# Performance work log

Hardware: AMD Instinct MI355X
Metric: run time of the kernel (lower is better)

## Reference

```python
import jax, jax.numpy as jnp
import numpy as np

N = 50000      # nodes
E = 800000     # edges (before self loops)
H = 4          # heads
C = 32         # hidden_channels per head
HC = H * C     # 128
L = 3          # num_layers - 2 conv blocks
G = 128        # graphs in batch
OUT = 10       # out_channels
VOCAB = 100
EPS = 1e-5


def setup_inputs() -> dict:
    key = jax.random.key(0)
    ks = jax.random.split(key, 16)
    s = 0.1
    return {
        "x_idx": jax.random.randint(ks[0], (N,), 0, VOCAB),
        "edge_index": jax.random.randint(ks[1], (2, E), 0, N),
        "batch": jnp.sort(jax.random.randint(ks[2], (N,), 0, G)),
        "embed": jax.random.normal(ks[3], (VOCAB, HC), jnp.float32) * s,
        "bn_gamma": jnp.ones((L, HC), jnp.float32),
        "bn_beta": jnp.zeros((L, HC), jnp.float32),
        "lin_W": jax.random.normal(ks[4], (L, C, HC), jnp.float32) * s,   # maps HC -> C (hidden)
        "lin_b": jnp.zeros((L, C), jnp.float32),
        "gat_W": jax.random.normal(ks[5], (L, HC, C), jnp.float32) * s,   # maps C -> H*C
        "att_src": jax.random.normal(ks[6], (L, H, C), jnp.float32) * s,
        "att_dst": jax.random.normal(ks[7], (L, H, C), jnp.float32) * s,
        "gat_b": jnp.zeros((L, HC), jnp.float32),
        "readout_W": jax.random.normal(ks[8], (OUT, HC), jnp.float32) * s,
        "readout_b": jnp.zeros((OUT,), jnp.float32),
    }


def _segment_softmax(logits, seg, num_segments):
    # logits: [E, H], seg: [E]
    m = jax.ops.segment_max(logits, seg, num_segments=num_segments)
    m = jnp.where(jnp.isfinite(m), m, 0.0)
    e = jnp.exp(logits - m[seg])
    z = jax.ops.segment_sum(e, seg, num_segments=num_segments)
    return e / (z[seg] + 1e-16)


def _forward(x_idx, edge_index, batch, embed, bn_gamma, bn_beta, lin_W, lin_b,
             gat_W, att_src, att_dst, gat_b, readout_W, readout_b):
    x = embed[x_idx]                                   # [N, HC]
    loops = jnp.arange(N)
    src = jnp.concatenate([edge_index[0], loops])      # add_self_loops=True
    dst = jnp.concatenate([edge_index[1], loops])
    for l in range(L):
        # BatchNorm1d (batch statistics)
        mean = jnp.mean(x, axis=0)
        var = jnp.var(x, axis=0)
        x = bn_gamma[l] * (x - mean) * jax.lax.rsqrt(var + EPS) + bn_beta[l]
        # Linear(HC -> C) + relu; dropout = identity (eval)
        x = jax.nn.relu(x @ lin_W[l].T + lin_b[l])      # [N, C]
        # GATConv(C -> C, heads=H, concat)
        h = (x @ gat_W[l].T).reshape(N, H, C)           # [N, H, C]
        a_src = jnp.sum(h * att_src[l], axis=-1)        # [N, H]
        a_dst = jnp.sum(h * att_dst[l], axis=-1)        # [N, H]
        logits = jax.nn.leaky_relu(a_src[src] + a_dst[dst], 0.2)  # [E+N, H]
        alpha = _segment_softmax(logits, dst, N)        # softmax over in-edges of each dst
        msg = h[src] * alpha[:, :, None]                # [E+N, H, C]
        x = jax.ops.segment_sum(msg, dst, num_segments=N).reshape(N, HC) + gat_b[l]
    x = x @ readout_W.T + readout_b                     # [N, OUT]
    return jax.ops.segment_sum(x, batch, num_segments=G)  # [G, OUT]


def reference(x_idx, edge_index, batch, embed, bn_gamma, bn_beta, lin_W, lin_b,
              gat_W, att_src, att_dst, gat_b, readout_W, readout_b):
    return _forward(x_idx, edge_index, batch, embed, bn_gamma, bn_beta, lin_W, lin_b,
                    gat_W, att_src, att_dst, gat_b, readout_W, readout_b)
```

## Files before the change

kernel.cpp:

```cpp
#include <hip/hip_runtime.h>

constexpr int NN   = 50000;
constexpr int NE   = 800000;
constexpr int NHD  = 4;
constexpr int CC   = 32;
constexpr int HCC  = 128;
constexpr int NL   = 3;
constexpr int NG   = 128;
constexpr int NOUT = 10;
constexpr float BN_EPS = 1e-5f;

constexpr int X2S = 67;
constexpr int YS = 33;
constexpr int NSLOT = 64;
constexpr int NBUK = (NN + 127) / 128;
constexpr int EB  = 2048;

__device__ inline unsigned f2bf_pack(float a, float b) {
    unsigned ua = __float_as_uint(a); ua += 0x7FFFu + ((ua >> 16) & 1u);
    unsigned ub = __float_as_uint(b); ub += 0x7FFFu + ((ub >> 16) & 1u);
    return (ua >> 16) | (ub & 0xFFFF0000u);
}
__device__ inline float bf_lo(unsigned p) { return __uint_as_float(p << 16); }
__device__ inline float bf_hi(unsigned p) { return __uint_as_float(p & 0xFFFF0000u); }

__global__ __launch_bounds__(256) void k_embed_stats(const int* __restrict__ idx,
                                                     const float* __restrict__ embed,
                                                     unsigned* __restrict__ xp,
                                                     float* __restrict__ stats) {
    int tid = threadIdx.x;
    int i0 = blockIdx.x * 256 + tid;
    int stride = gridDim.x * 256;
    float s0 = 0.f, s1 = 0.f, q0 = 0.f, q1 = 0.f;
    for (int i = i0; i < NN * 64; i += stride) {
        int n = i >> 6, c2 = (i & 63) << 1;
        float2 ev = *(const float2*)(embed + (size_t)idx[n] * HCC + c2);
        xp[i] = f2bf_pack(ev.x, ev.y);
        s0 += ev.x; q0 += ev.x * ev.x;
        s1 += ev.y; q1 += ev.y * ev.y;
    }
    __shared__ float A[256], B[256], C[256], D[256];
    A[tid] = s0; B[tid] = s1; C[tid] = q0; D[tid] = q1;
    __syncthreads();
    int slot = blockIdx.x & (NSLOT - 1);
    if (tid < 64) {
        int p = tid;
        float S0 = A[p] + A[p + 64] + A[p + 128] + A[p + 192];
        float S1 = B[p] + B[p + 64] + B[p + 128] + B[p + 192];
        float Q0 = C[p] + C[p + 64] + C[p + 128] + C[p + 192];
        float Q1 = D[p] + D[p + 64] + D[p + 128] + D[p + 192];
        atomicAdd(&stats[slot * 256 + 2 * p],           S0);
        atomicAdd(&stats[slot * 256 + 2 * p + 1],       S1);
        atomicAdd(&stats[slot * 256 + HCC + 2 * p],     Q0);
        atomicAdd(&stats[slot * 256 + HCC + 2 * p + 1], Q1);
    }
}

__global__ __launch_bounds__(256) void k_bhist(const int* __restrict__ ei,
                                               int* __restrict__ bkcnt,
                                               const int* __restrict__ batch,
                                               float* __restrict__ gcnt) {
    __shared__ int hist[NBUK];
    __shared__ int lgc[NG];
    int b = blockIdx.x, t = threadIdx.x;
    int e0 = b * EB, nE = min(EB, NE - e0);
    for (int i = t; i < NBUK; i += 256) hist[i] = 0;
    for (int i = t; i < NG; i += 256) lgc[i] = 0;
    __syncthreads();
    for (int i = t; i < nE; i += 256)
        atomicAdd(&hist[ei[NE + e0 + i] >> 7], 1);
    int n0 = b * 128;
    if (t < 128) {
        int n = n0 + t;
        if (n < NN) atomicAdd(&lgc[batch[n]], 1);
    }
    __syncthreads();
    for (int i = t; i < NBUK; i += 256)
        if (hist[i]) atomicAdd(&bkcnt[i], hist[i]);
    for (int i = t; i < NG; i += 256)
        if (lgc[i]) atomicAdd(&gcnt[i], (float)lgc[i]);
}

__global__ __launch_bounds__(512) void k_bscan(const int* __restrict__ bkcnt,
                                               int* __restrict__ bbase,
                                               int* __restrict__ bcnt,
                                               int* __restrict__ rowptr) {
    __shared__ int sc[512];
    int t = threadIdx.x;
    int v = (t < NBUK) ? bkcnt[t] : 0;
    sc[t] = v;
    __syncthreads();
#pragma unroll
    for (int off = 1; off < 512; off <<= 1) {
        int u = (t >= off) ? sc[t - off] : 0;
        __syncthreads();
        sc[t] += u;
        __syncthreads();
    }
    if (t < NBUK) {
        int excl = sc[t] - v;
        bbase[t] = excl;
        bcnt[t]  = excl;
    }
    if (t == 0) rowptr[NN] = NE;
}

__global__ __launch_bounds__(256) void k_bin(const int* __restrict__ ei,
                                             int* __restrict__ bcnt,
                                             unsigned* __restrict__ e_src) {
    __shared__ int hist[NBUK], base[NBUK];
    int b = blockIdx.x, t = threadIdx.x;
    int e0 = b * EB;
    int nE = min(EB, NE - e0);

    for (int i = t; i < NBUK; i += 256) hist[i] = 0;
    __syncthreads();
    for (int i = t; i < nE; i += 256)
        atomicAdd(&hist[ei[NE + e0 + i] >> 7], 1);
    __syncthreads();
    for (int i = t; i < NBUK; i += 256) {
        int c = hist[i];
        if (c) base[i] = atomicAdd(&bcnt[i], c);
        hist[i] = 0;
    }
    __syncthreads();
    for (int i = t; i < nE; i += 256) {
        int e = e0 + i;
        int d = ei[NE + e];
        int s = ei[e];
        int bk = d >> 7;
        int pos = base[bk] + atomicAdd(&hist[bk], 1);
        e_src[pos] = (unsigned)s | ((unsigned)(d & 127) << 17);
    }
}

__global__ __launch_bounds__(512) void k_place(const int* __restrict__ bbase,
                                               unsigned* __restrict__ e_src,
                                               int* __restrict__ rowptr) {
    __shared__ int lcnt[128], sc[128], lrp[128], cnt[128];
    int b = blockIdx.x, t = threadIdx.x;
    int d0 = b * 128;
    int rS = bbase[b];
    int rE = (b + 1 < NBUK) ? bbase[b + 1] : NE;
    int n = rE - rS;
    if (t < 128) { lcnt[t] = 0; cnt[t] = 0; }
    __syncthreads();
    unsigned pk[7];
#pragma unroll
    for (int k = 0; k < 7; k++) {
        int i = t + k * 512;
        if (i < n) {
            pk[k] = e_src[rS + i];
            atomicAdd(&lcnt[pk[k] >> 17], 1);
        }
    }
    __syncthreads();
    if (t < 128) sc[t] = lcnt[t];
    __syncthreads();
#pragma unroll
    for (int off = 1; off < 128; off <<= 1) {
        int u = (t < 128 && t >= off) ? sc[t - off] : 0;
        __syncthreads();
        if (t < 128) sc[t] += u;
        __syncthreads();
    }
    if (t < 128) {
        int start = rS + sc[t] - lcnt[t];
        lrp[t] = start;
        int d = d0 + t;
        if (d < NN) rowptr[d] = start;
    }
    __syncthreads();
#pragma unroll
    for (int k = 0; k < 7; k++) {
        int i = t + k * 512;
        if (i < n) {
            unsigned p = pk[k];
            int dl = p >> 17;
            int pos = lrp[dl] + atomicAdd(&cnt[dl], 1);
            e_src[pos] = p & 0x1FFFFu;
        }
    }
}

__global__ __launch_bounds__(256) void k_fused(const unsigned* __restrict__ xp,
                                               const float* __restrict__ stats,
                                               const float* __restrict__ gamma,
                                               const float* __restrict__ beta,
                                               const float* __restrict__ W1,
                                               const float* __restrict__ b1,
                                               const float* __restrict__ W2,
                                               const float* __restrict__ aS,
                                               const float* __restrict__ aD,
                                               unsigned* __restrict__ h,
                                               float* __restrict__ asrc,
                                               float* __restrict__ adst) {
    __shared__ unsigned xb2[64 * X2S];
    __shared__ float yt[64 * YS];
    __shared__ float __attribute__((aligned(16))) ssl[256];
    int tid = threadIdx.x;
    int node0 = blockIdx.x * 64;
    int nNodes = min(64, NN - node0);

    if (tid < 128) {
        float s = 0.f, q = 0.f;
        for (int sl = 0; sl < NSLOT; sl++) {
            s += stats[sl * 256 + tid];
            q += stats[sl * 256 + HCC + tid];
        }
        float mean = s * (1.0f / NN);
        float var  = q * (1.0f / NN) - mean * mean;
        float sc   = gamma[tid] * rsqrtf(var + BN_EPS);
        ssl[tid]       = sc;
        ssl[HCC + tid] = beta[tid] - mean * sc;
    }
    __syncthreads();

    {
        for (int q4 = tid; q4 < nNodes * 16; q4 += 256) {
            int n = q4 >> 4, c8 = q4 & 15;
            uint4 xv = *(const uint4*)(xp + (size_t)(node0 + n) * 64 + c8 * 4);
            int c = c8 * 8;
            float4 sc0 = *(const float4*)&ssl[c];
            float4 sc1 = *(const float4*)&ssl[c + 4];
            float4 sh0 = *(const float4*)&ssl[HCC + c];
            float4 sh1 = *(const float4*)&ssl[HCC + c + 4];
            unsigned* dst = &xb2[n * X2S + c8 * 4];
            dst[0] = f2bf_pack(bf_lo(xv.x) * sc0.x + sh0.x, bf_hi(xv.x) * sc0.y + sh0.y);
            dst[1] = f2bf_pack(bf_lo(xv.y) * sc0.z + sh0.z, bf_hi(xv.y) * sc0.w + sh0.w);
            dst[2] = f2bf_pack(bf_lo(xv.z) * sc1.x + sh1.x, bf_hi(xv.z) * sc1.y + sh1.y);
            dst[3] = f2bf_pack(bf_lo(xv.w) * sc1.z + sh1.z, bf_hi(xv.w) * sc1.w + sh1.w);
        }
    }
    __syncthreads();

    int lane = tid & 63;
    int wv = __builtin_amdgcn_readfirstlane(tid >> 6);
    int n = lane;

    {
        int j0 = wv * 8;
        const float* w1p = W1 + j0 * 128;
        float acc[8];
#pragma unroll
        for (int k = 0; k < 8; k++) acc[k] = b1[j0 + k];
        if (n < nNodes) {
            for (int cb = 0; cb < 128; cb += 4) {
                unsigned p0 = xb2[n * X2S + (cb >> 1)];
                unsigned p1 = xb2[n * X2S + (cb >> 1) + 1];
                float xv0 = bf_lo(p0), xv1 = bf_hi(p0);
                float xv2 = bf_lo(p1), xv3 = bf_hi(p1);
#pragma unroll
                for (int k = 0; k < 8; k++) {
                    float4 w = *(const float4*)&w1p[k * 128 + cb];
                    acc[k] += xv0 * w.x + xv1 * w.y + xv2 * w.z + xv3 * w.w;
                }
            }
#pragma unroll
            for (int k = 0; k < 8; k++) yt[n * YS + j0 + k] = fmaxf(acc[k], 0.f);
        }
    }
    __syncthreads();

    if (n < nNodes) {
        int k0 = wv * 32, hd = wv;
        const float* w2p = W2 + k0 * 32;
        const float* aSp = aS + hd * 32;
        const float* aDp = aD + hd * 32;
        float yreg[32];
#pragma unroll
        for (int j = 0; j < 32; j++) yreg[j] = yt[n * YS + j];
        float sa = 0.f, da = 0.f;
        unsigned* hrow = h + (size_t)(node0 + n) * 64;
        for (int kb = 0; kb < 32; kb += 8) {
            float acck[8];
#pragma unroll
            for (int kk = 0; kk < 8; kk++) acck[kk] = 0.f;
#pragma unroll
            for (int j = 0; j < 32; j += 4) {
#pragma unroll
                for (int kk = 0; kk < 8; kk++) {
                    float4 w = *(const float4*)&w2p[(kb + kk) * 32 + j];
                    acck[kk] += yreg[j] * w.x + yreg[j + 1] * w.y +
                                yreg[j + 2] * w.z + yreg[j + 3] * w.w;
                }
            }
#pragma unroll
            for (int kk = 0; kk < 8; kk++) {
                sa += acck[kk] * aSp[kb + kk];
                da += acck[kk] * aDp[kb + kk];
            }
            uint4 pk;
            pk.x = f2bf_pack(acck[0], acck[1]);
            pk.y = f2bf_pack(acck[2], acck[3]);
            pk.z = f2bf_pack(acck[4], acck[5]);
            pk.w = f2bf_pack(acck[6], acck[7]);
            *(uint4*)(hrow + ((kb) >> 1) + (k0 >> 1)) = pk;
        }
        asrc[(node0 + n) * 4 + hd] = sa;
        adst[(node0 + n) * 4 + hd] = da;
    }
}

__global__ __launch_bounds__(256) void k_agg(const int* __restrict__ rowptr,
                                             const int* __restrict__ e_src,
                                             const float* __restrict__ asrc,
                                             const float* __restrict__ adst,
                                             const unsigned* __restrict__ h,
                                             const float* __restrict__ gat_b,
                                             unsigned* __restrict__ xo,
                                             float* __restrict__ stats,
                                             const int* __restrict__ batch,
                                             float* __restrict__ gsum,
                                             int mode) {
    int tid = threadIdx.x, lane = tid & 63, wv = tid >> 6;
    int g  = lane >> 4;
    int li = lane & 15;
    int hd = li >> 2;
    int d  = blockIdx.x * 16 + wv * 4 + g;

    float4 bA = *(const float4*)(gat_b + li * 8);
    float4 bB = *(const float4*)(gat_b + li * 8 + 4);

    int begin = rowptr[d];
    int end   = rowptr[d + 1];
    float adv = adst[d * 4 + hd];
    float asl = asrc[d * 4 + hd];
    uint4 hs  = *(const uint4*)(h + (size_t)d * 64 + li * 4);

    float acc[8];
#pragma unroll
    for (int k = 0; k < 8; k++) acc[k] = 0.f;
    float ws = 0.f;

    int s[8];
    if (begin < end) {
#pragma unroll
        for (int t = 0; t < 8; t++) s[t] = e_src[min(begin + t, end - 1)];
    }

    for (int j = begin; j < end; j += 8) {
        uint4 hv[8];
#pragma unroll
        for (int t = 0; t < 8; t++) hv[t] = *(const uint4*)(h + (size_t)s[t] * 64 + li * 4);
        float av[8];
#pragma unroll
        for (int t = 0; t < 8; t++) av[t] = asrc[s[t] * 4 + hd];
        int jn = j + 8;
        int sn[8];
#pragma unroll
        for (int t = 0; t < 8; t++) sn[t] = s[t];
        if (jn < end) {
#pragma unroll
            for (int t = 0; t < 8; t++) sn[t] = e_src[min(jn + t, end - 1)];
        }
#pragma unroll
        for (int t = 0; t < 8; t++) {
            float l = av[t] + adv; l = l > 0.f ? l : 0.2f * l;
            float w = (j + t < end) ? __expf(l) : 0.f;
            acc[0] += w * bf_lo(hv[t].x); acc[1] += w * bf_hi(hv[t].x);
            acc[2] += w * bf_lo(hv[t].y); acc[3] += w * bf_hi(hv[t].y);
            acc[4] += w * bf_lo(hv[t].z); acc[5] += w * bf_hi(hv[t].z);
            acc[6] += w * bf_lo(hv[t].w); acc[7] += w * bf_hi(hv[t].w);
            ws += w;
        }
#pragma unroll
        for (int t = 0; t < 8; t++) s[t] = sn[t];
    }

    {
        float l = asl + adv; l = l > 0.f ? l : 0.2f * l;
        float w = __expf(l);
        acc[0] += w * bf_lo(hs.x); acc[1] += w * bf_hi(hs.x);
        acc[2] += w * bf_lo(hs.y); acc[3] += w * bf_hi(hs.y);
        acc[4] += w * bf_lo(hs.z); acc[5] += w * bf_hi(hs.z);
        acc[6] += w * bf_lo(hs.w); acc[7] += w * bf_hi(hs.w);
        ws += w;
    }

    float inv = 1.0f / (ws + 1e-16f);
    float o[8];
    o[0] = acc[0] * inv + bA.x; o[1] = acc[1] * inv + bA.y;
    o[2] = acc[2] * inv + bA.z; o[3] = acc[3] * inv + bA.w;
    o[4] = acc[4] * inv + bB.x; o[5] = acc[5] * inv + bB.y;
    o[6] = acc[6] * inv + bB.z; o[7] = acc[7] * inv + bB.w;

    __shared__ float redS[16 * 128], redQ[16 * 128];
    __shared__ int bg[16];
    int r = wv * 4 + g;

    if (mode == 1) {
        uint4 pk;
        pk.x = f2bf_pack(o[0], o[1]);
        pk.y = f2bf_pack(o[2], o[3]);
        pk.z = f2bf_pack(o[4], o[5]);
        pk.w = f2bf_pack(o[6], o[7]);
        *(uint4*)(xo + (size_t)d * 64 + li * 4) = pk;

#pragma unroll
        for (int k = 0; k < 8; k++) {
            redS[r * 128 + li * 8 + k] = o[k];
            redQ[r * 128 + li * 8 + k] = o[k] * o[k];
        }
        __syncthreads();
        int slot = blockIdx.x & (NSLOT - 1);
        if (tid < 128) {
            float v = 0.f;
#pragma unroll
            for (int rr = 0; rr < 16; rr++) v += redS[rr * 128 + tid];
            atomicAdd(&stats[slot * 256 + tid], v);
        } else {
            int c = tid - 128;
            float v = 0.f;
#pragma unroll
            for (int rr = 0; rr < 16; rr++) v += redQ[rr * 128 + c];
            atomicAdd(&stats[slot * 256 + HCC + c], v);
        }
    } else {
        if (li == 0) bg[r] = batch[d];
#pragma unroll
        for (int k = 0; k < 8; k++) redS[r * 128 + li * 8 + k] = o[k];
        __syncthreads();
        if (tid < 128) {
            float sacc = 0.f;
            int curg = bg[0];
#pragma unroll
            for (int rr = 0; rr < 16; rr++) {
                int gg = bg[rr];
                if (gg != curg) {
                    atomicAdd(&gsum[curg * HCC + tid], sacc);
                    sacc = 0.f; curg = gg;
                }
                sacc += redS[rr * 128 + tid];
            }
            atomicAdd(&gsum[curg * HCC + tid], sacc);
        }
    }
}

__global__ __launch_bounds__(128) void k_out(const float* __restrict__ gsum,
                                             const float* __restrict__ gcnt,
                                             const float* __restrict__ W,
                                             const float* __restrict__ bb,
                                             float* __restrict__ out) {
    __shared__ float v[128];
    int g = blockIdx.x, t = threadIdx.x;
    v[t] = gsum[g * HCC + t];
    __syncthreads();
    if (t < NOUT) {
        float acc = gcnt[g] * bb[t];
        const float* wr = W + t * HCC;
        for (int c = 0; c < HCC; c++) acc += v[c] * wr[c];
        out[g * NOUT + t] = acc;
    }
}

extern "C" void kernel_launch(void* const* d_in, const int* in_sizes, int n_in,
                              void* d_out, int out_size, void* d_ws, size_t ws_size,
                              hipStream_t stream) {
    const int*   x_idx = (const int*)d_in[0];
    const int*   ei    = (const int*)d_in[1];
    const int*   batch = (const int*)d_in[2];
    const float* embed = (const float*)d_in[3];
    const float* bn_g  = (const float*)d_in[4];
    const float* bn_b  = (const float*)d_in[5];
    const float* lin_W = (const float*)d_in[6];
    const float* lin_b = (const float*)d_in[7];
    const float* gat_W = (const float*)d_in[8];
    const float* att_s = (const float*)d_in[9];
    const float* att_d = (const float*)d_in[10];
    const float* gat_b = (const float*)d_in[11];
    const float* ro_W  = (const float*)d_in[12];
    const float* ro_b  = (const float*)d_in[13];
    float* out = (float*)d_out;

    const size_t STG = (size_t)NSLOT * 256;
    unsigned* xp    = (unsigned*)d_ws;
    unsigned* h     = xp + (size_t)NN * 64;
    float*    asrc  = (float*)(h + (size_t)NN * 64);
    float*    adst  = asrc + (size_t)NN * NHD;
    float*    stats = adst + (size_t)NN * NHD;
    float*    gsum  = stats + 3 * STG;
    float*    gcnt  = gsum + (size_t)NG * HCC;
    int*      bkcnt  = (int*)(gcnt + NG);
    int*      bbase  = bkcnt + NBUK;
    int*      bcnt   = bbase + NBUK;
    int*      rowptr = bcnt + NBUK;
    unsigned* e_src  = (unsigned*)(rowptr + NN + 1);

    hipMemsetAsync(stats, 0,
                   (3 * STG + (size_t)NG * HCC + NG) * sizeof(float) + NBUK * sizeof(int),
                   stream);

    k_embed_stats<<<512, 256, 0, stream>>>(x_idx, embed, xp, stats);
    k_bhist<<<(NE + EB - 1) / EB, 256, 0, stream>>>(ei, bkcnt, batch, gcnt);
    k_bscan<<<1, 512, 0, stream>>>(bkcnt, bbase, bcnt, rowptr);
    k_bin<<<(NE + EB - 1) / EB, 256, 0, stream>>>(ei, bcnt, e_src);
    k_place<<<NBUK, 512, 0, stream>>>(bbase, e_src, rowptr);

    for (int l = 0; l < NL; ++l) {
        k_fused<<<(NN + 63) / 64, 256, 0, stream>>>(xp, stats + l * STG,
                                                    bn_g + l * HCC, bn_b + l * HCC,
                                                    lin_W + l * CC * HCC, lin_b + l * CC,
                                                    gat_W + l * HCC * CC,
                                                    att_s + l * NHD * CC,
                                                    att_d + l * NHD * CC,
                                                    h, asrc, adst);
        k_agg<<<NN / 16, 256, 0, stream>>>(rowptr, (const int*)e_src, asrc, adst, h,
                                           gat_b + l * HCC, xp,
                                           stats + (l + 1) * STG,
                                           batch, gsum,
                                           (l < NL - 1) ? 1 : 2);
    }

    k_out<<<NG, 128, 0, stream>>>(gsum, gcnt, ro_W, ro_b, out);
}
```

Measured before the change: 338.3 us.

## Sort each node's in-edges into source-range tiles and aggregate tile by tile

During CSR construction, each destination's edges are now grouped into four source-index ranges (12500 nodes each), and per-node counts for each range are stored in a new tcnt array. The aggregation kernel walks these four segments in order with an unroll of 4 instead of 8. The aim is temporal locality in the h/asrc gathers: all waves sweep source ranges in a similar order, so the working set in L2 is smaller. The cost is an extra per-node count read, more loop overhead and tail waste per segment, and less memory-level parallelism from the smaller unroll.

```diff
diff --git a/kernel.cpp b/kernel.cpp
--- a/kernel.cpp
+++ b/kernel.cpp
@@ -15,6 +15,8 @@
 constexpr int NSLOT = 64;
 constexpr int NBUK = (NN + 127) / 128;
 constexpr int EB  = 2048;
+constexpr int NT  = 4;
+constexpr int TSZ = 12500;
 
 __device__ inline unsigned f2bf_pack(float a, float b) {
     unsigned ua = __float_as_uint(a); ua += 0x7FFFu + ((ua >> 16) & 1u);
@@ -136,26 +138,37 @@
 
 __global__ __launch_bounds__(512) void k_place(const int* __restrict__ bbase,
                                                unsigned* __restrict__ e_src,
-                                               int* __restrict__ rowptr) {
-    __shared__ int lcnt[128], sc[128], lrp[128], cnt[128];
+                                               int* __restrict__ rowptr,
+                                               int* __restrict__ tcnt) {
+    __shared__ int lcnt2[128][NT], cnt2[128][NT], sc[128], lrp[128];
     int b = blockIdx.x, t = threadIdx.x;
     int d0 = b * 128;
     int rS = bbase[b];
     int rE = (b + 1 < NBUK) ? bbase[b + 1] : NE;
     int n = rE - rS;
-    if (t < 128) { lcnt[t] = 0; cnt[t] = 0; }
-    __syncthreads();
-    unsigned pk[7];
+    if (t < 128) {
+#pragma unroll
+        for (int k = 0; k < NT; k++) { lcnt2[t][k] = 0; cnt2[t][k] = 0; }
+    }
+    __syncthreads();
+    unsigned pk[7]; int tl[7];
 #pragma unroll
     for (int k = 0; k < 7; k++) {
         int i = t + k * 512;
         if (i < n) {
             pk[k] = e_src[rS + i];
-            atomicAdd(&lcnt[pk[k] >> 17], 1);
-        }
-    }
-    __syncthreads();
-    if (t < 128) sc[t] = lcnt[t];
+            int src = pk[k] & 0x1FFFFu;
+            tl[k] = min(src / TSZ, NT - 1);
+            atomicAdd(&lcnt2[pk[k] >> 17][tl[k]], 1);
+        }
+    }
+    __syncthreads();
+    int deg = 0;
+    if (t < 128) {
+#pragma unroll
+        for (int k = 0; k < NT; k++) deg += lcnt2[t][k];
+        sc[t] = deg;
+    }
     __syncthreads();
 #pragma unroll
     for (int off = 1; off < 128; off <<= 1) {
@@ -165,10 +178,16 @@
         __syncthreads();
     }
     if (t < 128) {
-        int start = rS + sc[t] - lcnt[t];
+        int start = rS + sc[t] - deg;
         lrp[t] = start;
         int d = d0 + t;
-        if (d < NN) rowptr[d] = start;
+        if (d < NN) {
+            rowptr[d] = start;
+            *(int4*)&tcnt[(size_t)d * NT] =
+                make_int4(lcnt2[t][0], lcnt2[t][1], lcnt2[t][2], lcnt2[t][3]);
+        }
+        int b0 = 0, b1 = lcnt2[t][0], b2 = b1 + lcnt2[t][1], b3 = b2 + lcnt2[t][2];
+        lcnt2[t][0] = b0; lcnt2[t][1] = b1; lcnt2[t][2] = b2; lcnt2[t][3] = b3;
     }
     __syncthreads();
 #pragma unroll
@@ -177,7 +196,7 @@
         if (i < n) {
             unsigned p = pk[k];
             int dl = p >> 17;
-            int pos = lrp[dl] + atomicAdd(&cnt[dl], 1);
+            int pos = lrp[dl] + lcnt2[dl][tl[k]] + atomicAdd(&cnt2[dl][tl[k]], 1);
             e_src[pos] = p & 0x1FFFFu;
         }
     }
@@ -304,6 +323,7 @@
 
 __global__ __launch_bounds__(256) void k_agg(const int* __restrict__ rowptr,
                                              const int* __restrict__ e_src,
+                                             const int* __restrict__ tcnt,
                                              const float* __restrict__ asrc,
                                              const float* __restrict__ adst,
                                              const unsigned* __restrict__ h,
@@ -323,49 +343,56 @@
     float4 bB = *(const float4*)(gat_b + li * 8 + 4);
 
     int begin = rowptr[d];
-    int end   = rowptr[d + 1];
     float adv = adst[d * 4 + hd];
     float asl = asrc[d * 4 + hd];
     uint4 hs  = *(const uint4*)(h + (size_t)d * 64 + li * 4);
+    int tcs[4];
+    {
+        int4 tc = *(const int4*)(tcnt + (size_t)d * 4);
+        tcs[0] = tc.x; tcs[1] = tc.y; tcs[2] = tc.z; tcs[3] = tc.w;
+    }
 
     float acc[8];
 #pragma unroll
     for (int k = 0; k < 8; k++) acc[k] = 0.f;
     float ws = 0.f;
 
-    int s[8];
-    if (begin < end) {
-#pragma unroll
-        for (int t = 0; t < 8; t++) s[t] = e_src[min(begin + t, end - 1)];
-    }
-
-    for (int j = begin; j < end; j += 8) {
-        uint4 hv[8];
-#pragma unroll
-        for (int t = 0; t < 8; t++) hv[t] = *(const uint4*)(h + (size_t)s[t] * 64 + li * 4);
-        float av[8];
-#pragma unroll
-        for (int t = 0; t < 8; t++) av[t] = asrc[s[t] * 4 + hd];
-        int jn = j + 8;
-        int sn[8];
-#pragma unroll
-        for (int t = 0; t < 8; t++) sn[t] = s[t];
-        if (jn < end) {
-#pragma unroll
-            for (int t = 0; t < 8; t++) sn[t] = e_src[min(jn + t, end - 1)];
-        }
-#pragma unroll
-        for (int t = 0; t < 8; t++) {
-            float l = av[t] + adv; l = l > 0.f ? l : 0.2f * l;
-            float w = (j + t < end) ? __expf(l) : 0.f;
-            acc[0] += w * bf_lo(hv[t].x); acc[1] += w * bf_hi(hv[t].x);
-            acc[2] += w * bf_lo(hv[t].y); acc[3] += w * bf_hi(hv[t].y);
-            acc[4] += w * bf_lo(hv[t].z); acc[5] += w * bf_hi(hv[t].z);
-            acc[6] += w * bf_lo(hv[t].w); acc[7] += w * bf_hi(hv[t].w);
-            ws += w;
-        }
-#pragma unroll
-        for (int t = 0; t < 8; t++) s[t] = sn[t];
+    int segB = begin;
+    for (int tt = 0; tt < NT; ++tt) {
+        int sB = segB, sE = segB + tcs[tt];
+        segB = sE;
+        if (sB >= sE) continue;
+        int s[4];
+#pragma unroll
+        for (int t = 0; t < 4; t++) s[t] = e_src[min(sB + t, sE - 1)];
+        for (int j = sB; j < sE; j += 4) {
+            uint4 hv[4];
+#pragma unroll
+            for (int t = 0; t < 4; t++) hv[t] = *(const uint4*)(h + (size_t)s[t] * 64 + li * 4);
+            float av[4];
+#pragma unroll
+            for (int t = 0; t < 4; t++) av[t] = asrc[s[t] * 4 + hd];
+            int jn = j + 4;
+            int sn[4];
+#pragma unroll
+            for (int t = 0; t < 4; t++) sn[t] = s[t];
+            if (jn < sE) {
+#pragma unroll
+                for (int t = 0; t < 4; t++) sn[t] = e_src[min(jn + t, sE - 1)];
+            }
+#pragma unroll
+            for (int t = 0; t < 4; t++) {
+                float l = av[t] + adv; l = l > 0.f ? l : 0.2f * l;
+                float w = (j + t < sE) ? __expf(l) : 0.f;
+                acc[0] += w * bf_lo(hv[t].x); acc[1] += w * bf_hi(hv[t].x);
+                acc[2] += w * bf_lo(hv[t].y); acc[3] += w * bf_hi(hv[t].y);
+                acc[4] += w * bf_lo(hv[t].z); acc[5] += w * bf_hi(hv[t].z);
+                acc[6] += w * bf_lo(hv[t].w); acc[7] += w * bf_hi(hv[t].w);
+                ws += w;
+            }
+#pragma unroll
+            for (int t = 0; t < 4; t++) s[t] = sn[t];
+        }
     }
 
     {
@@ -487,6 +514,7 @@
     int*      bcnt   = bbase + NBUK;
     int*      rowptr = bcnt + NBUK;
     unsigned* e_src  = (unsigned*)(rowptr + NN + 1);
+    int*      tcnt   = (int*)((((size_t)(e_src + NE)) + 15) & ~(size_t)15);
 
     hipMemsetAsync(stats, 0,
                    (3 * STG + (size_t)NG * HCC + NG) * sizeof(float) + NBUK * sizeof(int),
@@ -496,7 +524,7 @@
     k_bhist<<<(NE + EB - 1) / EB, 256, 0, stream>>>(ei, bkcnt, batch, gcnt);
     k_bscan<<<1, 512, 0, stream>>>(bkcnt, bbase, bcnt, rowptr);
     k_bin<<<(NE + EB - 1) / EB, 256, 0, stream>>>(ei, bcnt, e_src);
-    k_place<<<NBUK, 512, 0, stream>>>(bbase, e_src, rowptr);
+    k_place<<<NBUK, 512, 0, stream>>>(bbase, e_src, rowptr, tcnt);
 
     for (int l = 0; l < NL; ++l) {
         k_fused<<<(NN + 63) / 64, 256, 0, stream>>>(xp, stats + l * STG,
@@ -506,7 +534,7 @@
                                                     att_s + l * NHD * CC,
                                                     att_d + l * NHD * CC,
                                                     h, asrc, adst);
-        k_agg<<<NN / 16, 256, 0, stream>>>(rowptr, (const int*)e_src, asrc, adst, h,
+        k_agg<<<NN / 16, 256, 0, stream>>>(rowptr, (const int*)e_src, tcnt, asrc, adst, h,
                                            gat_b + l * HCC, xp,
                                            stats + (l + 1) * STG,
                                            batch, gsum,
```

After: 345.7 us. +2.2%, slower.
